# Kernel tuning notes

Measured on AMD Instinct MI355X. Metric: run time of the kernel, lower is better.

Reference implementation:

```python
import jax, jax.numpy as jnp
import numpy as np

N = 50000      # nodes
E = 800000     # edges (avg degree 16)
F_IN = 128     # input feature dim
HID = 64       # hidden_channels
HEADS = 2
NEG_SLOPE = 0.2


def setup_inputs() -> dict:
    key = jax.random.key(0)
    ks = jax.random.split(key, 20)
    w = lambda k, shape: jax.random.normal(k, shape, jnp.float32) * 0.1
    inp = {
        "x": jax.random.normal(ks[0], (N, F_IN), jnp.float32),
        "edge_index": jax.random.randint(ks[1], (2, E), 0, N, dtype=jnp.int32),
    }
    # layer specs: (in_dim, heads) ; out per head = HID
    specs = [(F_IN, HEADS), (HID * HEADS, HEADS), (HID * HEADS, HEADS), (HID * HEADS, 1)]
    ki = 2
    for i, (fin, h) in enumerate(specs, 1):
        inp[f"Wl{i}"] = w(ks[ki], (fin, h * HID)); ki += 1
        inp[f"Wr{i}"] = w(ks[ki], (fin, h * HID)); ki += 1
        inp[f"att{i}"] = w(ks[ki], (h, HID)); ki += 1
        inp[f"b{i}"] = jnp.zeros((h * HID,), jnp.float32)
    return inp


def gat_layer(x, src, dst, Wl, Wr, att, b):
    # GATv2Conv: e_ij = att . LeakyReLU(Wl x_j + Wr x_i), softmax over incoming edges of i
    H, C = att.shape
    n = x.shape[0]
    xl = (x @ Wl).reshape(n, H, C)   # source-side transform
    xr = (x @ Wr).reshape(n, H, C)   # target-side transform
    e = jax.nn.leaky_relu(xl[src] + xr[dst], negative_slope=NEG_SLOPE)  # [E,H,C]
    score = jnp.einsum('ehc,hc->eh', e, att)                            # [E,H]
    # segment softmax over destination nodes
    m = jax.ops.segment_max(score, dst, num_segments=n)
    m = jnp.where(jnp.isfinite(m), m, 0.0)  # nodes with no in-edges
    ex = jnp.exp(score - m[dst])
    den = jax.ops.segment_sum(ex, dst, num_segments=n)
    alpha = ex / (den[dst] + 1e-16)                                     # [E,H]
    out = jax.ops.segment_sum(xl[src] * alpha[:, :, None], dst, num_segments=n)  # [N,H,C]
    return out.reshape(n, H * C) + b


def reference(x, edge_index, Wl1, Wr1, att1, b1, Wl2, Wr2, att2, b2,
              Wl3, Wr3, att3, b3, Wl4, Wr4, att4, b4):
    src, dst = edge_index[0], edge_index[1]
    x = jax.nn.relu(gat_layer(x, src, dst, Wl1, Wr1, att1, b1))
    x = jax.nn.relu(gat_layer(x, src, dst, Wl2, Wr2, att2, b2))
    x = jax.nn.relu(gat_layer(x, src, dst, Wl3, Wr3, att3, b3))
    return gat_layer(x, src, dst, Wl4, Wr4, att4, b4)  # [N, HID]
```

## Files before the change

kernel.cpp:

```cpp
#include <hip/hip_runtime.h>
#include <hip/hip_fp16.h>
#include <math.h>
#include <limits.h>

#define FIN 128
#define NEG_SLOPE 0.2f

typedef _Float16 f16x8 __attribute__((ext_vector_type(8)));
typedef float f32x4 __attribute__((ext_vector_type(4)));
typedef float f32x2 __attribute__((ext_vector_type(2)));

static __device__ __forceinline__ f32x2 pk_add(f32x2 a, f32x2 b) {
    f32x2 d; asm("v_pk_add_f32 %0, %1, %2" : "=v"(d) : "v"(a), "v"(b)); return d;
}
static __device__ __forceinline__ f32x2 pk_fma(f32x2 a, f32x2 b, f32x2 c) {
    f32x2 d; asm("v_pk_fma_f32 %0, %1, %2, %3" : "=v"(d) : "v"(a), "v"(b), "v"(c)); return d;
}

static __device__ __forceinline__ f32x2 h2f2x(unsigned int u) {
    __half2 h = *reinterpret_cast<__half2*>(&u);
    float2 f = __half22float2(h);
    return (f32x2){f.x, f.y};
}

template <int CTRL>
static __device__ __forceinline__ float dpp_add(float x) {
    int t = __builtin_amdgcn_update_dpp(0, __builtin_bit_cast(int, x), CTRL, 0xF, 0xF, true);
    return x + __builtin_bit_cast(float, t);
}
static __device__ __forceinline__ float reduce8_dpp(float p) {
    p = dpp_add<0xB1>(p);
    p = dpp_add<0x4E>(p);
    p = dpp_add<0x141>(p);
    return p;
}


__global__ void k_hist_part(const int* __restrict__ dst, int* __restrict__ counts,
                            int E, int span) {
    const int r = blockIdx.x & 7;
    const int chunk = blockIdx.x >> 3;
    const int nchunks = gridDim.x >> 3;
    const int lo = r * span, hi = lo + span;
    const int per = (E + nchunks - 1) / nchunks;
    const int e1 = min(E, (chunk + 1) * per);
    for (int e = chunk * per + threadIdx.x; e < e1; e += blockDim.x) {
        int d = dst[e];
        if (d >= lo && d < hi) atomicAdd(&counts[d], 1);
    }
}

__global__ void k_scatter_part(const int* __restrict__ dst, const int* __restrict__ rowptr,
                               int* __restrict__ nfill, int* __restrict__ colids,
                               int E, int span) {
    const int r = blockIdx.x & 7;
    const int chunk = blockIdx.x >> 3;
    const int nchunks = gridDim.x >> 3;
    const int lo = r * span, hi = lo + span;
    const int per = (E + nchunks - 1) / nchunks;
    const int e1 = min(E, (chunk + 1) * per);
    for (int e = chunk * per + threadIdx.x; e < e1; e += blockDim.x) {
        int d = dst[e];
        if (d >= lo && d < hi) {
            int pos = atomicAdd(&nfill[d], 1);
            colids[rowptr[d] + pos] = e;
        }
    }
}

__global__ void k_scan1(const int* __restrict__ counts, int* __restrict__ incl,
                        int* __restrict__ partial, int n) {
    __shared__ int tmp[1024];
    int tid = threadIdx.x, base = blockIdx.x * 1024;
    int v = (base + tid < n) ? counts[base + tid] : 0;
    tmp[tid] = v;
    __syncthreads();
    for (int off = 1; off < 1024; off <<= 1) {
        int t = (tid >= off) ? tmp[tid - off] : 0;
        __syncthreads();
        tmp[tid] += t;
        __syncthreads();
    }
    if (base + tid < n) incl[base + tid] = tmp[tid];
    if (tid == 1023) partial[blockIdx.x] = tmp[1023];
}

__global__ void k_scan3(const int* __restrict__ counts, const int* __restrict__ incl,
                        const int* __restrict__ partial, int* __restrict__ rowptr,
                        int* __restrict__ nfill, int n, int nb) {
    __shared__ int sbase;
    if (threadIdx.x == 0) {
        int b = 0;
        for (int p = 0; p < (int)blockIdx.x; ++p) b += partial[p];
        sbase = b;
        if ((int)blockIdx.x == nb - 1) {
            int tot = b;
            for (int p = blockIdx.x; p < nb; ++p) tot += partial[p];
            rowptr[n] = tot;
        }
    }
    __syncthreads();
    int i = blockIdx.x * 1024 + threadIdx.x;
    if (i < n) {
        rowptr[i] = sbase + incl[i] - counts[i];
        nfill[i] = 0;
    }
}

__global__ void k_sort(const int* __restrict__ rowptr, const int* __restrict__ colids,
                       const int* __restrict__ esrc, int* __restrict__ colsrc, int n) {
    int node = blockIdx.x * 4 + (threadIdx.x >> 6);
    int lane = threadIdx.x & 63;
    if (node >= n) return;
    int s = rowptr[node], e = rowptr[node + 1];
    int d = e - s;
    if (d <= 0) return;
    if (d <= 64) {
        int v = (lane < d) ? colids[s + lane] : INT_MAX;
        int rank = 0;
        for (int j = 0; j < d; ++j) {
            int vj = __shfl(v, j, 64);
            rank += (vj < v) ? 1 : 0;
        }
        if (lane < d) colsrc[s + rank] = esrc[v];
    } else {
        if (lane == 0) {
            int last = -1;
            for (int k = 0; k < d; ++k) {
                int best = INT_MAX;
                for (int j = s; j < e; ++j) {
                    int id = colids[j];
                    if (id > last && id < best) best = id;
                }
                colsrc[s + k] = esrc[best];
                last = best;
            }
        }
    }
}


struct WprepArgs {
    const float* Wl[4];
    const float* Wr[4];
    __half* Wz[4];
};

__global__ void k_wprep_all(WprepArgs a) {
    int b = blockIdx.x;
    int layer = (b < 16) ? 0 : (b < 32) ? 1 : (b < 48) ? 2 : 3;
    int base = layer * 16;
    int HC = (layer == 3) ? 64 : 128;
    int NT = 2 * HC / 16;
    int tid = (b - base) * 256 + threadIdx.x;
    int l = tid & 63, c = tid >> 6;
    int ks = c / NT, nt = c % NT;
    int col = nt * 16 + (l & 15);
    int kbase = ks * 32 + ((l >> 4) << 3);
    const float* W = (col < HC) ? (a.Wl[layer] + col) : (a.Wr[layer] + (col - HC));
    __half h[8];
#pragma unroll
    for (int j = 0; j < 8; ++j) h[j] = __float2half(W[(size_t)(kbase + j) * HC]);
    *(uint4*)&a.Wz[layer][(size_t)tid * 8] = *(const uint4*)h;
}


template <int HC, bool CVT>
__global__ void __launch_bounds__(256) k_gemm_mfma(
        const void* __restrict__ Ain, const __half* __restrict__ Wz,
        __half* __restrict__ xl, float* __restrict__ xr, int n) {
    constexpr int NT = 2 * HC / 16;
    const int l = threadIdx.x & 63;
    const int wid = threadIdx.x >> 6;
    const int r0 = (blockIdx.x * 4 + wid) * 16;
    if (r0 >= n) return;
    const int m = l & 15, kb = l >> 4;
    const int ra = min(r0 + m, n - 1);
    const f16x8* Bz = (const f16x8*)Wz;

    f32x4 acc[NT];
#pragma unroll
    for (int nt = 0; nt < NT; ++nt) acc[nt] = (f32x4){0.f, 0.f, 0.f, 0.f};

#pragma unroll
    for (int ks = 0; ks < 4; ++ks) {
        f16x8 a;
        if (CVT) {
            const float* Af = (const float*)Ain + (size_t)ra * FIN + kb * 8 + ks * 32;
            float4 f0 = *(const float4*)Af;
            float4 f1 = *(const float4*)(Af + 4);
            a[0] = (_Float16)f0.x; a[1] = (_Float16)f0.y;
            a[2] = (_Float16)f0.z; a[3] = (_Float16)f0.w;
            a[4] = (_Float16)f1.x; a[5] = (_Float16)f1.y;
            a[6] = (_Float16)f1.z; a[7] = (_Float16)f1.w;
        } else {
            a = *(const f16x8*)((const _Float16*)Ain + (size_t)ra * FIN + kb * 8 + ks * 32);
        }
#pragma unroll
        for (int nt = 0; nt < NT; ++nt) {
            f16x8 b = Bz[(ks * NT + nt) * 64 + l];
            acc[nt] = __builtin_amdgcn_mfma_f32_16x16x32_f16(a, b, acc[nt], 0, 0, 0);
        }
    }

    const int rb = r0 + kb * 4;
#pragma unroll
    for (int nt = 0; nt < NT; ++nt) {
        int c = nt * 16 + m;
        if (nt < NT / 2) {
#pragma unroll
            for (int r = 0; r < 4; ++r) {
                int row = rb + r;
                if (row < n) xl[(size_t)row * HC + c] = __float2half(acc[nt][r]);
            }
        } else {
            int cd = c - HC;
#pragma unroll
            for (int r = 0; r < 4; ++r) {
                int row = rb + r;
                if (row < n) xr[(size_t)row * HC + cd] = acc[nt][r];
            }
        }
    }
}


template <bool RELU>
__global__ void __launch_bounds__(256) k_fused2(
        const __half* __restrict__ xlh, const float* __restrict__ xr,
        const int* __restrict__ rowptr, const int* __restrict__ colsrc,
        const float* __restrict__ attc, const float* __restrict__ bias,
        __half* __restrict__ out, int N) {
    const int lane = threadIdx.x & 63;
    const int g = lane >> 4;
    const int s = lane & 15;
    const int c0 = s * 8;
    int i = blockIdx.x * 4 + (threadIdx.x >> 6);
    const int stride = gridDim.x * 4;
    const float L2E = 1.4426950408889634f;

    f32x2 a6[4], a4[4];
    {
        float4 a0 = *(const float4*)&attc[c0];
        float4 a1 = *(const float4*)&attc[c0 + 4];
        float t[8] = {a0.x, a0.y, a0.z, a0.w, a1.x, a1.y, a1.z, a1.w};
#pragma unroll
        for (int k = 0; k < 4; ++k) {
            a6[k] = (f32x2){0.6f * L2E * t[2 * k], 0.6f * L2E * t[2 * k + 1]};
            a4[k] = (f32x2){0.4f * L2E * t[2 * k], 0.4f * L2E * t[2 * k + 1]};
        }
    }

    if (i >= N) return;
    int st = rowptr[i];
    int en = rowptr[i + 1];
    int c0i = colsrc[st + g];
    int c1i = colsrc[st + 4 + g];
    int c2i = colsrc[st + 8 + g];
    int c3i = colsrc[st + 12 + g];
    int p0 = colsrc[st + 16 + g];
    int p1 = colsrc[st + 20 + g];

    while (true) {
        const int inext = i + stride;
        int nst = 0, nen = 0;
        if (inext < N) {
            nst = rowptr[inext];
            nen = rowptr[inext + 1];
        }
        f32x2 xrv[4];
        {
            float4 r0 = *(const float4*)&xr[(size_t)i * 128 + c0];
            float4 r1 = *(const float4*)&xr[(size_t)i * 128 + c0 + 4];
            xrv[0] = (f32x2){r0.x, r0.y}; xrv[1] = (f32x2){r0.z, r0.w};
            xrv[2] = (f32x2){r1.x, r1.y}; xrv[3] = (f32x2){r1.z, r1.w};
        }
        uint4 w0 = *(const uint4*)(xlh + ((size_t)c0i << 7) + c0);
        uint4 w1 = *(const uint4*)(xlh + ((size_t)c1i << 7) + c0);
        uint4 w2 = *(const uint4*)(xlh + ((size_t)c2i << 7) + c0);
        uint4 w3 = *(const uint4*)(xlh + ((size_t)c3i << 7) + c0);
        int i0 = p0, i1 = p1;

        float den = 0.f;
        f32x2 acc[4];
#pragma unroll
        for (int k = 0; k < 4; ++k) acc[k] = (f32x2){0.f, 0.f};

        for (int j = st; j < en; j += 8) {
            uint4 n0 = *(const uint4*)(xlh + ((size_t)i0 << 7) + c0);
            uint4 n1 = *(const uint4*)(xlh + ((size_t)i1 << 7) + c0);
            i0 = colsrc[j + 24 + g];
            i1 = colsrc[j + 28 + g];

#pragma unroll
            for (int q = 0; q < 2; ++q) {
                const uint4 w = q ? w1 : w0;
                f32x2 xv[4];
                xv[0] = h2f2x(w.x); xv[1] = h2f2x(w.y);
                xv[2] = h2f2x(w.z); xv[3] = h2f2x(w.w);
                f32x2 sc = (f32x2){0.f, 0.f};
#pragma unroll
                for (int k = 0; k < 4; ++k) {
                    f32x2 u = pk_add(xv[k], xrv[k]);
                    sc = pk_fma(u, a6[k], sc);
                    f32x2 ua = {__builtin_fabsf(u.x), __builtin_fabsf(u.y)};
                    sc = pk_fma(ua, a4[k], sc);
                }
                float p = reduce8_dpp(sc.x + sc.y);
                p = (j + q * 4 + g < en) ? p : -INFINITY;
                float pe = exp2f(p);
                den += pe;
                f32x2 pe2 = (f32x2){pe, pe};
#pragma unroll
                for (int k = 0; k < 4; ++k) acc[k] = pk_fma(pe2, xv[k], acc[k]);
            }
            w0 = w2; w1 = w3; w2 = n0; w3 = n1;
        }

        if (inext < N) {
            c0i = colsrc[nst + g];
            c1i = colsrc[nst + 4 + g];
            c2i = colsrc[nst + 8 + g];
            c3i = colsrc[nst + 12 + g];
            p0 = colsrc[nst + 16 + g];
            p1 = colsrc[nst + 20 + g];
        }

#pragma unroll
        for (int off = 16; off <= 32; off <<= 1) {
            den += __shfl_xor(den, off, 64);
#pragma unroll
            for (int k = 0; k < 4; ++k) {
                acc[k].x += __shfl_xor(acc[k].x, off, 64);
                acc[k].y += __shfl_xor(acc[k].y, off, 64);
            }
        }

        if (g == 0) {
            float4 b0 = *(const float4*)&bias[c0];
            float4 b1 = *(const float4*)&bias[c0 + 4];
            float bv[8] = {b0.x, b0.y, b0.z, b0.w, b1.x, b1.y, b1.z, b1.w};
            float inv = 1.f / (den + 1e-16f);
            __half hb[8];
#pragma unroll
            for (int k = 0; k < 8; ++k) {
                float av = (k & 1) ? acc[k >> 1].y : acc[k >> 1].x;
                float o = fmaf(av, inv, bv[k]);
                if (RELU) o = fmaxf(o, 0.f);
                hb[k] = __float2half(o);
            }
            *(uint4*)&out[(size_t)i * 128 + c0] = *(const uint4*)hb;
        }

        if (inext >= N) break;
        i = inext; st = nst; en = nen;
    }
}


__global__ void __launch_bounds__(256) k_fused1(
        const __half* __restrict__ xlh, const float* __restrict__ xr,
        const int* __restrict__ rowptr, const int* __restrict__ colsrc,
        const float* __restrict__ attc, const float* __restrict__ bias,
        float* __restrict__ out, int N) {
    const int lane = threadIdx.x & 63;
    const int g = lane >> 3;
    const int s = lane & 7;
    const int c0 = s * 8;
    int i = blockIdx.x * 4 + (threadIdx.x >> 6);
    const int stride = gridDim.x * 4;
    const float L2E = 1.4426950408889634f;

    f32x2 a6[4], a4[4];
    {
        float4 a0 = *(const float4*)&attc[c0];
        float4 a1 = *(const float4*)&attc[c0 + 4];
        float t[8] = {a0.x, a0.y, a0.z, a0.w, a1.x, a1.y, a1.z, a1.w};
#pragma unroll
        for (int k = 0; k < 4; ++k) {
            a6[k] = (f32x2){0.6f * L2E * t[2 * k], 0.6f * L2E * t[2 * k + 1]};
            a4[k] = (f32x2){0.4f * L2E * t[2 * k], 0.4f * L2E * t[2 * k + 1]};
        }
    }

    if (i >= N) return;
    int st = rowptr[i];
    int en = rowptr[i + 1];
    int c0i = colsrc[st + g];
    int c1i = colsrc[st + 8 + g];
    int p0 = colsrc[st + 16 + g];
    int p1 = colsrc[st + 24 + g];

    while (true) {
        const int inext = i + stride;
        int nst = 0, nen = 0;
        if (inext < N) {
            nst = rowptr[inext];
            nen = rowptr[inext + 1];
        }
        f32x2 xrv[4];
        {
            float4 r0 = *(const float4*)&xr[(size_t)i * 64 + c0];
            float4 r1 = *(const float4*)&xr[(size_t)i * 64 + c0 + 4];
            xrv[0] = (f32x2){r0.x, r0.y}; xrv[1] = (f32x2){r0.z, r0.w};
            xrv[2] = (f32x2){r1.x, r1.y}; xrv[3] = (f32x2){r1.z, r1.w};
        }
        uint4 w0 = *(const uint4*)(xlh + ((size_t)c0i << 6) + c0);
        uint4 w1 = *(const uint4*)(xlh + ((size_t)c1i << 6) + c0);
        int i0 = p0, i1 = p1;

        float den = 0.f;
        f32x2 acc[4];
#pragma unroll
        for (int k = 0; k < 4; ++k) acc[k] = (f32x2){0.f, 0.f};

        for (int j = st; j < en; j += 16) {
            uint4 n0 = *(const uint4*)(xlh + ((size_t)i0 << 6) + c0);
            uint4 n1 = *(const uint4*)(xlh + ((size_t)i1 << 6) + c0);
            i0 = colsrc[j + 32 + g];
            i1 = colsrc[j + 40 + g];

#pragma unroll
            for (int q = 0; q < 2; ++q) {
                const uint4 w = q ? w1 : w0;
                f32x2 xv[4];
                xv[0] = h2f2x(w.x); xv[1] = h2f2x(w.y);
                xv[2] = h2f2x(w.z); xv[3] = h2f2x(w.w);
                f32x2 sc = (f32x2){0.f, 0.f};
#pragma unroll
                for (int k = 0; k < 4; ++k) {
                    f32x2 u = pk_add(xv[k], xrv[k]);
                    sc = pk_fma(u, a6[k], sc);
                    f32x2 ua = {__builtin_fabsf(u.x), __builtin_fabsf(u.y)};
                    sc = pk_fma(ua, a4[k], sc);
                }
                float p = reduce8_dpp(sc.x + sc.y);
                p = (j + q * 8 + g < en) ? p : -INFINITY;
                float pe = exp2f(p);
                den += pe;
                f32x2 pe2 = (f32x2){pe, pe};
#pragma unroll
                for (int k = 0; k < 4; ++k) acc[k] = pk_fma(pe2, xv[k], acc[k]);
            }
            w0 = n0; w1 = n1;
        }

        if (inext < N) {
            c0i = colsrc[nst + g];
            c1i = colsrc[nst + 8 + g];
            p0 = colsrc[nst + 16 + g];
            p1 = colsrc[nst + 24 + g];
        }

#pragma unroll
        for (int off = 8; off <= 32; off <<= 1) {
            den += __shfl_xor(den, off, 64);
#pragma unroll
            for (int k = 0; k < 4; ++k) {
                acc[k].x += __shfl_xor(acc[k].x, off, 64);
                acc[k].y += __shfl_xor(acc[k].y, off, 64);
            }
        }

        if (g == 0) {
            float4 b0 = *(const float4*)&bias[c0];
            float4 b1 = *(const float4*)&bias[c0 + 4];
            float bv[8] = {b0.x, b0.y, b0.z, b0.w, b1.x, b1.y, b1.z, b1.w};
            float inv = 1.f / (den + 1e-16f);
            float o[8];
#pragma unroll
            for (int k = 0; k < 8; ++k) {
                float av = (k & 1) ? acc[k >> 1].y : acc[k >> 1].x;
                o[k] = fmaf(av, inv, bv[k]);
            }
            *(float4*)&out[(size_t)i * 64 + c0] = make_float4(o[0], o[1], o[2], o[3]);
            *(float4*)&out[(size_t)i * 64 + c0 + 4] = make_float4(o[4], o[5], o[6], o[7]);
        }

        if (inext >= N) break;
        i = inext; st = nst; en = nen;
    }
}


static inline size_t align_up(size_t v, size_t a) { return (v + a - 1) & ~(a - 1); }

extern "C" void kernel_launch(void* const* d_in, const int* in_sizes, int n_in,
                              void* d_out, int out_size, void* d_ws, size_t ws_size,
                              hipStream_t stream) {
    const float* x = (const float*)d_in[0];
    const int* ei = (const int*)d_in[1];
    const int N = in_sizes[0] / FIN;
    const int E = in_sizes[1] / 2;
    const int* esrc = ei;
    const int* edst = ei + E;

    const float* Wl1 = (const float*)d_in[2];
    const float* Wr1 = (const float*)d_in[3];
    const float* att1 = (const float*)d_in[4];
    const float* b1 = (const float*)d_in[5];
    const float* Wl2 = (const float*)d_in[6];
    const float* Wr2 = (const float*)d_in[7];
    const float* att2 = (const float*)d_in[8];
    const float* b2 = (const float*)d_in[9];
    const float* Wl3 = (const float*)d_in[10];
    const float* Wr3 = (const float*)d_in[11];
    const float* att3 = (const float*)d_in[12];
    const float* b3 = (const float*)d_in[13];
    const float* Wl4 = (const float*)d_in[14];
    const float* Wr4 = (const float*)d_in[15];
    const float* att4 = (const float*)d_in[16];
    const float* b4 = (const float*)d_in[17];

    const int nb = (N + 1023) / 1024;
    const int span = (N + 7) / 8;

    size_t off = 0;
    char* w = (char*)d_ws;
    auto alloc = [&](size_t bytes) {
        char* p = w + off;
        off = align_up(off + bytes, 256);
        return p;
    };
    int* rowptr = (int*)alloc((size_t)(N + 1) * 4);
    int* nfill = (int*)alloc((size_t)N * 4);
    int* incl = (int*)alloc((size_t)N * 4);
    int* partial = (int*)alloc(1024 * 4);
    int* colids = (int*)alloc((size_t)E * 4);
    int* colsrc = (int*)alloc((size_t)(E + 64) * 4);
    __half* xb16 = (__half*)alloc((size_t)N * FIN * 2);
    __half* xlh = (__half*)alloc((size_t)N * FIN * 2);
    float* xr = (float*)alloc((size_t)N * FIN * 4);
    __half* Wz1 = (__half*)alloc(65536);
    __half* Wz2 = (__half*)alloc(65536);
    __half* Wz3 = (__half*)alloc(65536);
    __half* Wz4 = (__half*)alloc(32768);
    if (off > ws_size) return;

    hipMemsetAsync(nfill, 0, (size_t)N * 4, stream);
    hipMemsetAsync(colsrc + E, 0, 64 * 4, stream);
    k_hist_part<<<2048, 256, 0, stream>>>(edst, nfill, E, span);
    k_scan1<<<nb, 1024, 0, stream>>>(nfill, incl, partial, N);
    k_scan3<<<nb, 1024, 0, stream>>>(nfill, incl, partial, rowptr, nfill, N, nb);
    k_scatter_part<<<2048, 256, 0, stream>>>(edst, rowptr, nfill, colids, E, span);
    k_sort<<<(N + 3) / 4, 256, 0, stream>>>(rowptr, colids, esrc, colsrc, N);

    WprepArgs wa;
    wa.Wl[0] = Wl1; wa.Wl[1] = Wl2; wa.Wl[2] = Wl3; wa.Wl[3] = Wl4;
    wa.Wr[0] = Wr1; wa.Wr[1] = Wr2; wa.Wr[2] = Wr3; wa.Wr[3] = Wr4;
    wa.Wz[0] = Wz1; wa.Wz[1] = Wz2; wa.Wz[2] = Wz3; wa.Wz[3] = Wz4;
    k_wprep_all<<<56, 256, 0, stream>>>(wa);

    const int gg = (N + 63) / 64;
    const int gf = 2048;

    k_gemm_mfma<128, true><<<gg, 256, 0, stream>>>(x, Wz1, xlh, xr, N);
    k_fused2<true><<<gf, 256, 0, stream>>>(xlh, xr, rowptr, colsrc, att1, b1, xb16, N);
    k_gemm_mfma<128, false><<<gg, 256, 0, stream>>>(xb16, Wz2, xlh, xr, N);
    k_fused2<true><<<gf, 256, 0, stream>>>(xlh, xr, rowptr, colsrc, att2, b2, xb16, N);
    k_gemm_mfma<128, false><<<gg, 256, 0, stream>>>(xb16, Wz3, xlh, xr, N);
    k_fused2<true><<<gf, 256, 0, stream>>>(xlh, xr, rowptr, colsrc, att3, b3, xb16, N);
    k_gemm_mfma<64, false><<<gg, 256, 0, stream>>>(xb16, Wz4, xlh, xr, N);
    k_fused1<<<gf, 256, 0, stream>>>(xlh, xr, rowptr, colsrc, att4, b4, (float*)d_out, N);
}
```

Measured before the change: 380.4 us.

## Split two-head layers into per-head fp16 buffers and run per-head aggregation

The GEMM now writes source and target features into separate 64-wide per-head fp16 buffers, and xr is stored as fp16 instead of fp32. The two-head fused aggregation kernel is removed. Each two-head layer instead runs the single-head kernel twice, once per head, writing into strided halves of the output. This aims to shrink the per-head gather working set so it fits in cache better and to halve xr traffic, at the cost of extra launches, reading the CSR twice and lower xr precision.

```diff
diff --git a/kernel.cpp b/kernel.cpp
--- a/kernel.cpp
+++ b/kernel.cpp
@@ -4,7 +4,6 @@
 #include <limits.h>
 
 #define FIN 128
-#define NEG_SLOPE 0.2f
 
 typedef _Float16 f16x8 __attribute__((ext_vector_type(8)));
 typedef float f32x4 __attribute__((ext_vector_type(4)));
@@ -168,7 +167,8 @@
 template <int HC, bool CVT>
 __global__ void __launch_bounds__(256) k_gemm_mfma(
         const void* __restrict__ Ain, const __half* __restrict__ Wz,
-        __half* __restrict__ xl, float* __restrict__ xr, int n) {
+        __half* __restrict__ xl0, __half* __restrict__ xl1,
+        __half* __restrict__ xr0, __half* __restrict__ xr1, int n) {
     constexpr int NT = 2 * HC / 16;
     const int l = threadIdx.x & 63;
     const int wid = threadIdx.x >> 6;
@@ -206,163 +206,33 @@
     const int rb = r0 + kb * 4;
 #pragma unroll
     for (int nt = 0; nt < NT; ++nt) {
-        int c = nt * 16 + m;
-        if (nt < NT / 2) {
-#pragma unroll
-            for (int r = 0; r < 4; ++r) {
-                int row = rb + r;
-                if (row < n) xl[(size_t)row * HC + c] = __float2half(acc[nt][r]);
-            }
+        int col = nt * 16 + m;
+        __half* dst;
+        int ch;
+        if (HC == 128) {
+            if (nt < 4)       { dst = xl0; ch = col; }
+            else if (nt < 8)  { dst = xl1; ch = col - 64; }
+            else if (nt < 12) { dst = xr0; ch = col - 128; }
+            else              { dst = xr1; ch = col - 192; }
         } else {
-            int cd = c - HC;
-#pragma unroll
-            for (int r = 0; r < 4; ++r) {
-                int row = rb + r;
-                if (row < n) xr[(size_t)row * HC + cd] = acc[nt][r];
-            }
-        }
-    }
-}
-
-
-template <bool RELU>
-__global__ void __launch_bounds__(256) k_fused2(
-        const __half* __restrict__ xlh, const float* __restrict__ xr,
+            if (nt < 4) { dst = xl0; ch = col; }
+            else        { dst = xr0; ch = col - 64; }
+        }
+#pragma unroll
+        for (int r = 0; r < 4; ++r) {
+            int row = rb + r;
+            if (row < n) dst[(size_t)row * 64 + ch] = __float2half(acc[nt][r]);
+        }
+    }
+}
+
+
+template <bool F16OUT, bool RELU>
+__global__ void __launch_bounds__(256) k_fused_h(
+        const __half* __restrict__ xlh, const __half* __restrict__ xrh,
         const int* __restrict__ rowptr, const int* __restrict__ colsrc,
         const float* __restrict__ attc, const float* __restrict__ bias,
-        __half* __restrict__ out, int N) {
-    const int lane = threadIdx.x & 63;
-    const int g = lane >> 4;
-    const int s = lane & 15;
-    const int c0 = s * 8;
-    int i = blockIdx.x * 4 + (threadIdx.x >> 6);
-    const int stride = gridDim.x * 4;
-    const float L2E = 1.4426950408889634f;
-
-    f32x2 a6[4], a4[4];
-    {
-        float4 a0 = *(const float4*)&attc[c0];
-        float4 a1 = *(const float4*)&attc[c0 + 4];
-        float t[8] = {a0.x, a0.y, a0.z, a0.w, a1.x, a1.y, a1.z, a1.w};
-#pragma unroll
-        for (int k = 0; k < 4; ++k) {
-            a6[k] = (f32x2){0.6f * L2E * t[2 * k], 0.6f * L2E * t[2 * k + 1]};
-            a4[k] = (f32x2){0.4f * L2E * t[2 * k], 0.4f * L2E * t[2 * k + 1]};
-        }
-    }
-
-    if (i >= N) return;
-    int st = rowptr[i];
-    int en = rowptr[i + 1];
-    int c0i = colsrc[st + g];
-    int c1i = colsrc[st + 4 + g];
-    int c2i = colsrc[st + 8 + g];
-    int c3i = colsrc[st + 12 + g];
-    int p0 = colsrc[st + 16 + g];
-    int p1 = colsrc[st + 20 + g];
-
-    while (true) {
-        const int inext = i + stride;
-        int nst = 0, nen = 0;
-        if (inext < N) {
-            nst = rowptr[inext];
-            nen = rowptr[inext + 1];
-        }
-        f32x2 xrv[4];
-        {
-            float4 r0 = *(const float4*)&xr[(size_t)i * 128 + c0];
-            float4 r1 = *(const float4*)&xr[(size_t)i * 128 + c0 + 4];
-            xrv[0] = (f32x2){r0.x, r0.y}; xrv[1] = (f32x2){r0.z, r0.w};
-            xrv[2] = (f32x2){r1.x, r1.y}; xrv[3] = (f32x2){r1.z, r1.w};
-        }
-        uint4 w0 = *(const uint4*)(xlh + ((size_t)c0i << 7) + c0);
-        uint4 w1 = *(const uint4*)(xlh + ((size_t)c1i << 7) + c0);
-        uint4 w2 = *(const uint4*)(xlh + ((size_t)c2i << 7) + c0);
-        uint4 w3 = *(const uint4*)(xlh + ((size_t)c3i << 7) + c0);
-        int i0 = p0, i1 = p1;
-
-        float den = 0.f;
-        f32x2 acc[4];
-#pragma unroll
-        for (int k = 0; k < 4; ++k) acc[k] = (f32x2){0.f, 0.f};
-
-        for (int j = st; j < en; j += 8) {
-            uint4 n0 = *(const uint4*)(xlh + ((size_t)i0 << 7) + c0);
-            uint4 n1 = *(const uint4*)(xlh + ((size_t)i1 << 7) + c0);
-            i0 = colsrc[j + 24 + g];
-            i1 = colsrc[j + 28 + g];
-
-#pragma unroll
-            for (int q = 0; q < 2; ++q) {
-                const uint4 w = q ? w1 : w0;
-                f32x2 xv[4];
-                xv[0] = h2f2x(w.x); xv[1] = h2f2x(w.y);
-                xv[2] = h2f2x(w.z); xv[3] = h2f2x(w.w);
-                f32x2 sc = (f32x2){0.f, 0.f};
-#pragma unroll
-                for (int k = 0; k < 4; ++k) {
-                    f32x2 u = pk_add(xv[k], xrv[k]);
-                    sc = pk_fma(u, a6[k], sc);
-                    f32x2 ua = {__builtin_fabsf(u.x), __builtin_fabsf(u.y)};
-                    sc = pk_fma(ua, a4[k], sc);
-                }
-                float p = reduce8_dpp(sc.x + sc.y);
-                p = (j + q * 4 + g < en) ? p : -INFINITY;
-                float pe = exp2f(p);
-                den += pe;
-                f32x2 pe2 = (f32x2){pe, pe};
-#pragma unroll
-                for (int k = 0; k < 4; ++k) acc[k] = pk_fma(pe2, xv[k], acc[k]);
-            }
-            w0 = w2; w1 = w3; w2 = n0; w3 = n1;
-        }
-
-        if (inext < N) {
-            c0i = colsrc[nst + g];
-            c1i = colsrc[nst + 4 + g];
-            c2i = colsrc[nst + 8 + g];
-            c3i = colsrc[nst + 12 + g];
-            p0 = colsrc[nst + 16 + g];
-            p1 = colsrc[nst + 20 + g];
-        }
-
-#pragma unroll
-        for (int off = 16; off <= 32; off <<= 1) {
-            den += __shfl_xor(den, off, 64);
-#pragma unroll
-            for (int k = 0; k < 4; ++k) {
-                acc[k].x += __shfl_xor(acc[k].x, off, 64);
-                acc[k].y += __shfl_xor(acc[k].y, off, 64);
-            }
-        }
-
-        if (g == 0) {
-            float4 b0 = *(const float4*)&bias[c0];
-            float4 b1 = *(const float4*)&bias[c0 + 4];
-            float bv[8] = {b0.x, b0.y, b0.z, b0.w, b1.x, b1.y, b1.z, b1.w};
-            float inv = 1.f / (den + 1e-16f);
-            __half hb[8];
-#pragma unroll
-            for (int k = 0; k < 8; ++k) {
-                float av = (k & 1) ? acc[k >> 1].y : acc[k >> 1].x;
-                float o = fmaf(av, inv, bv[k]);
-                if (RELU) o = fmaxf(o, 0.f);
-                hb[k] = __float2half(o);
-            }
-            *(uint4*)&out[(size_t)i * 128 + c0] = *(const uint4*)hb;
-        }
-
-        if (inext >= N) break;
-        i = inext; st = nst; en = nen;
-    }
-}
-
-
-__global__ void __launch_bounds__(256) k_fused1(
-        const __half* __restrict__ xlh, const float* __restrict__ xr,
-        const int* __restrict__ rowptr, const int* __restrict__ colsrc,
-        const float* __restrict__ attc, const float* __restrict__ bias,
-        float* __restrict__ out, int N) {
+        void* __restrict__ outp, int orow, int N) {
     const int lane = threadIdx.x & 63;
     const int g = lane >> 3;
     const int s = lane & 7;
@@ -400,10 +270,9 @@
         }
         f32x2 xrv[4];
         {
-            float4 r0 = *(const float4*)&xr[(size_t)i * 64 + c0];
-            float4 r1 = *(const float4*)&xr[(size_t)i * 64 + c0 + 4];
-            xrv[0] = (f32x2){r0.x, r0.y}; xrv[1] = (f32x2){r0.z, r0.w};
-            xrv[2] = (f32x2){r1.x, r1.y}; xrv[3] = (f32x2){r1.z, r1.w};
+            uint4 rw = *(const uint4*)&xrh[(size_t)i * 64 + c0];
+            xrv[0] = h2f2x(rw.x); xrv[1] = h2f2x(rw.y);
+            xrv[2] = h2f2x(rw.z); xrv[3] = h2f2x(rw.w);
         }
         uint4 w0 = *(const uint4*)(xlh + ((size_t)c0i << 6) + c0);
         uint4 w1 = *(const uint4*)(xlh + ((size_t)c1i << 6) + c0);
@@ -467,14 +336,28 @@
             float4 b1 = *(const float4*)&bias[c0 + 4];
             float bv[8] = {b0.x, b0.y, b0.z, b0.w, b1.x, b1.y, b1.z, b1.w};
             float inv = 1.f / (den + 1e-16f);
-            float o[8];
-#pragma unroll
-            for (int k = 0; k < 8; ++k) {
-                float av = (k & 1) ? acc[k >> 1].y : acc[k >> 1].x;
-                o[k] = fmaf(av, inv, bv[k]);
+            if (F16OUT) {
+                __half hb[8];
+#pragma unroll
+                for (int k = 0; k < 8; ++k) {
+                    float av = (k & 1) ? acc[k >> 1].y : acc[k >> 1].x;
+                    float o = fmaf(av, inv, bv[k]);
+                    if (RELU) o = fmaxf(o, 0.f);
+                    hb[k] = __float2half(o);
+                }
+                *(uint4*)((__half*)outp + (size_t)i * orow + c0) = *(const uint4*)hb;
+            } else {
+                float o[8];
+#pragma unroll
+                for (int k = 0; k < 8; ++k) {
+                    float av = (k & 1) ? acc[k >> 1].y : acc[k >> 1].x;
+                    o[k] = fmaf(av, inv, bv[k]);
+                    if (RELU) o[k] = fmaxf(o[k], 0.f);
+                }
+                float* op = (float*)outp + (size_t)i * orow + c0;
+                *(float4*)op = make_float4(o[0], o[1], o[2], o[3]);
+                *(float4*)(op + 4) = make_float4(o[4], o[5], o[6], o[7]);
             }
-            *(float4*)&out[(size_t)i * 64 + c0] = make_float4(o[0], o[1], o[2], o[3]);
-            *(float4*)&out[(size_t)i * 64 + c0 + 4] = make_float4(o[4], o[5], o[6], o[7]);
         }
 
         if (inext >= N) break;
@@ -529,8 +412,10 @@
     int* colids = (int*)alloc((size_t)E * 4);
     int* colsrc = (int*)alloc((size_t)(E + 64) * 4);
     __half* xb16 = (__half*)alloc((size_t)N * FIN * 2);
-    __half* xlh = (__half*)alloc((size_t)N * FIN * 2);
-    float* xr = (float*)alloc((size_t)N * FIN * 4);
+    __half* xl0 = (__half*)alloc((size_t)N * 64 * 2);
+    __half* xl1 = (__half*)alloc((size_t)N * 64 * 2);
+    __half* xr0 = (__half*)alloc((size_t)N * 64 * 2);
+    __half* xr1 = (__half*)alloc((size_t)N * 64 * 2);
     __half* Wz1 = (__half*)alloc(65536);
     __half* Wz2 = (__half*)alloc(65536);
     __half* Wz3 = (__half*)alloc(65536);
@@ -554,12 +439,15 @@
     const int gg = (N + 63) / 64;
     const int gf = 2048;
 
-    k_gemm_mfma<128, true><<<gg, 256, 0, stream>>>(x, Wz1, xlh, xr, N);
-    k_fused2<true><<<gf, 256, 0, stream>>>(xlh, xr, rowptr, colsrc, att1, b1, xb16, N);
-    k_gemm_mfma<128, false><<<gg, 256, 0, stream>>>(xb16, Wz2, xlh, xr, N);
-    k_fused2<true><<<gf, 256, 0, stream>>>(xlh, xr, rowptr, colsrc, att2, b2, xb16, N);
-    k_gemm_mfma<128, false><<<gg, 256, 0, stream>>>(xb16, Wz3, xlh, xr, N);
-    k_fused2<true><<<gf, 256, 0, stream>>>(xlh, xr, rowptr, colsrc, att3, b3, xb16, N);
-    k_gemm_mfma<64, false><<<gg, 256, 0, stream>>>(xb16, Wz4, xlh, xr, N);
-    k_fused1<<<gf, 256, 0, stream>>>(xlh, xr, rowptr, colsrc, att4, b4, (float*)d_out, N);
-}
+    k_gemm_mfma<128, true><<<gg, 256, 0, stream>>>(x, Wz1, xl0, xl1, xr0, xr1, N);
+    k_fused_h<true, true><<<gf, 256, 0, stream>>>(xl0, xr0, rowptr, colsrc, att1, b1, xb16, 128, N);
+    k_fused_h<true, true><<<gf, 256, 0, stream>>>(xl1, xr1, rowptr, colsrc, att1 + 64, b1 + 64, xb16 + 64, 128, N);
+    k_gemm_mfma<128, false><<<gg, 256, 0, stream>>>(xb16, Wz2, xl0, xl1, xr0, xr1, N);
+    k_fused_h<true, true><<<gf, 256, 0, stream>>>(xl0, xr0, rowptr, colsrc, att2, b2, xb16, 128, N);
+    k_fused_h<true, true><<<gf, 256, 0, stream>>>(xl1, xr1, rowptr, colsrc, att2 + 64, b2 + 64, xb16 + 64, 128, N);
+    k_gemm_mfma<128, false><<<gg, 256, 0, stream>>>(xb16, Wz3, xl0, xl1, xr0, xr1, N);
+    k_fused_h<true, true><<<gf, 256, 0, stream>>>(xl0, xr0, rowptr, colsrc, att3, b3, xb16, 128, N);
+    k_fused_h<true, true><<<gf, 256, 0, stream>>>(xl1, xr1, rowptr, colsrc, att3 + 64, b3 + 64, xb16 + 64, 128, N);
+    k_gemm_mfma<64, false><<<gg, 256, 0, stream>>>(xb16, Wz4, xl0, nullptr, xr0, nullptr, N);
+    k_fused_h<false, false><<<gf, 256, 0, stream>>>(xl0, xr0, rowptr, colsrc, att4, b4, d_out, 64, N);
+}
```

Result: slower. 452.4 us (+18.9%).
